# Kernel optimization log

Measured on AMD Instinct MI355X. Metric: run time of the kernel, lower is better.

## Reference

```python
import jax, jax.numpy as jnp
import numpy as np

EPS = 1e-6  # matches torch nn.CosineSimilarity(eps=1e-6)

B, D, N, K = 128, 512, 500000, 3


def setup_inputs() -> dict:
    key = jax.random.key(0)
    k1, k2, k3 = jax.random.split(key, 3)
    query_r = jax.random.normal(k1, (B, D), dtype=jnp.float32)
    corpus_emb = jax.random.normal(k2, (N, D), dtype=jnp.float32)
    # stand-in for self.retriever.model.forward (projection to embedding space)
    W = jax.random.normal(k3, (D, D), dtype=jnp.float32) / np.sqrt(D)
    return {"query_r": query_r, "corpus_emb": corpus_emb, "W": W, "k": K}


def _l2_normalize(x):
    # torch CosineSimilarity clamps the norm at eps, not norm+eps
    n = jnp.sqrt(jnp.sum(x * x, axis=-1, keepdims=True))
    return x / jnp.maximum(n, EPS)


def reference(query_r, corpus_emb, W, k):
    # retriever projection: query = retriever.model.forward(query_r)
    query = query_r @ W                      # [B, D]
    qn = _l2_normalize(query)                # [B, D]
    cn = _l2_normalize(corpus_emb)           # [N, D]
    # fused replacement for the per-item python-loop cosine scan
    scores = jnp.einsum('bd,nd->bn', qn, cn)  # [B, N]
    # sort(reverse=True)[:k]  ==  top-k
    top_scores, top_idx = jax.lax.top_k(scores, k)  # [B, k], [B, k]
    return top_scores, top_idx
```

## Files before the change

kernel.cpp:

```cpp
#include <hip/hip_runtime.h>
#include <math.h>

#define B_Q   128
#define DIM   512
#define NCORP 500000
#define NTILES 31250
#define G_SCAN 512

typedef short short8 __attribute__((ext_vector_type(8)));
typedef float floatx4 __attribute__((ext_vector_type(4)));

__device__ __forceinline__ unsigned short bf16_rne(float x) {
    unsigned u = __float_as_uint(x);
    return (unsigned short)((u + 0x7FFFu + ((u >> 16) & 1u)) >> 16);
}

__device__ __forceinline__ unsigned pack2(float hi, float lo) {
    return __builtin_amdgcn_perm(__float_as_uint(hi), __float_as_uint(lo),
                                 0x07060302u);
}

__device__ __forceinline__ void ins3(float s, int id,
                                     float& b0, float& b1, float& b2,
                                     int& i0, int& i1, int& i2) {
    if (s > b0)      { b2 = b1; i2 = i1; b1 = b0; i1 = i0; b0 = s; i0 = id; }
    else if (s > b1) { b2 = b1; i2 = i1; b1 = s;  i1 = id; }
    else if (s > b2) { b2 = s;  i2 = id; }
}

__device__ __forceinline__ void ins2(float s, int id,
                                     float& b0, float& b1, int& i0, int& i1) {
    if (s > b0)      { b1 = b0; i1 = i0; b0 = s; i0 = id; }
    else if (s > b1) { b1 = s;  i1 = id; }
}

__device__ __forceinline__ void ins8(float s, int id, float* bs, int* bi) {
#pragma unroll
    for (int j = 0; j < 8; ++j) {
        if (s > bs[j]) {
            float tf = bs[j]; int tx = bi[j];
            bs[j] = s; bi[j] = id; s = tf; id = tx;
        }
    }
}

__global__ void proj_kernel(const float* __restrict__ qr,
                            const float* __restrict__ W,
                            float* __restrict__ qn,
                            unsigned short* __restrict__ qfrag) {
    __shared__ float qrow[DIM];
    __shared__ float red[256];
    const int b = blockIdx.x;
    const int t = threadIdx.x;

    qrow[t]       = qr[b * DIM + t];
    qrow[t + 256] = qr[b * DIM + t + 256];
    __syncthreads();

    float acc0 = 0.f, acc1 = 0.f;
#pragma unroll 8
    for (int k = 0; k < DIM; ++k) {
        const float q = qrow[k];
        acc0 = fmaf(q, W[k * DIM + t],       acc0);
        acc1 = fmaf(q, W[k * DIM + t + 256], acc1);
    }

    red[t] = acc0 * acc0 + acc1 * acc1;
    __syncthreads();
    for (int s = 128; s > 0; s >>= 1) {
        if (t < s) red[t] += red[t + s];
        __syncthreads();
    }
    const float inv = 1.0f / fmaxf(sqrtf(red[0]), 1e-6f);

    const int qg = b >> 4, q15 = b & 15;
#pragma unroll
    for (int half = 0; half < 2; ++half) {
        const int d = t + half * 256;
        const float x = (half == 0 ? acc0 : acc1) * inv;
        qn[b * DIM + d] = x;
        const int kc = d >> 5, kk = d & 31, g = kk >> 3, e = kk & 7;
        qfrag[(size_t)kc * 4096 + qg * 512 + (g * 16 + q15) * 8 + e] = bf16_rne(x);
    }
}

__global__ __launch_bounds__(512, 4) void scan_kernel(
        const float* __restrict__ corpus,
        const unsigned short* __restrict__ qfrag,
        float* __restrict__ cand_s,
        int*   __restrict__ cand_i) {
    __shared__ __align__(16) unsigned char smem[32768];

    const int t = threadIdx.x;
    const int w = t >> 6, l = t & 63;
    const int h = l >> 4, q15 = l & 15;

    short8 qreg[16];
#pragma unroll
    for (int kc = 0; kc < 16; ++kc)
        qreg[kc] = *(const short8*)(qfrag + (size_t)kc * 4096 + w * 512 + l * 8);

    int goff[4], lby[4];
#pragma unroll
    for (int p = 0; p < 4; ++p) {
        const int i4 = p * 512 + t;
        const int r  = i4 >> 7;
        const int c4 = i4 & 127;
        const int kc = c4 >> 3, g = (c4 >> 1) & 3, e0 = (c4 & 1) * 4;
        goff[p] = i4 * 4;
        lby[p]  = kc * 1024 + (((g * 16 + r) ^ (kc & 7)) << 4) + e0 * 2;
    }

    const int b = blockIdx.x;
    const int tstart = b * 61 + (b < 18 ? b : 18);
    const int tcount = 61 + (b < 18 ? 1 : 0);
    const float* seg = corpus + (size_t)tstart * 8192;

    float ts0 = -1e30f, ts1 = -1e30f;
    int   ti0 = 0, ti1 = 0;

    float4 rr[4];
#pragma unroll
    for (int p = 0; p < 4; ++p) rr[p] = *(const float4*)(seg + goff[p]);

#pragma unroll 1
    for (int T = 0; T < tcount; ++T) {
        unsigned char* bb = smem + (T & 1) * 16384;

#pragma unroll
        for (int p = 0; p < 4; ++p) {
            uint2 d;
            d.x = pack2(rr[p].y, rr[p].x);
            d.y = pack2(rr[p].w, rr[p].z);
            *(uint2*)(bb + lby[p]) = d;
        }
        {
            const int Tn = (T + 1 < tcount) ? T + 1 : T;
            const float* src = seg + (size_t)Tn * 8192;
#pragma unroll
            for (int p = 0; p < 4; ++p) rr[p] = *(const float4*)(src + goff[p]);
        }
        __builtin_amdgcn_sched_barrier(0);
        asm volatile("s_waitcnt lgkmcnt(0)" ::: "memory");
        __builtin_amdgcn_s_barrier();
        __builtin_amdgcn_sched_barrier(0);

        floatx4 acc  = {0.f, 0.f, 0.f, 0.f};
        floatx4 accN = {0.f, 0.f, 0.f, 0.f};
#pragma unroll
        for (int kc = 0; kc < 16; ++kc) {
            const short8 a = *(const short8*)(bb + kc * 1024 +
                                              ((l ^ (kc & 7)) << 4));
            accN = __builtin_amdgcn_mfma_f32_16x16x32_bf16(a, a, accN, 0, 0, 0);
            acc  = __builtin_amdgcn_mfma_f32_16x16x32_bf16(a, qreg[kc], acc, 0, 0, 0);
        }

        const int grow = (tstart + T) * 16;
#pragma unroll
        for (int reg = 0; reg < 4; ++reg) {
            const float nrm = __shfl(accN[reg], h * 20 + reg, 64);
            const float inv = 1.0f / fmaxf(sqrtf(nrm), 1e-6f);
            ins2(acc[reg] * inv, grow + h * 4 + reg, ts0, ts1, ti0, ti1);
        }
    }

    __syncthreads();
    float* msc = (float*)smem;
    int*   mid = (int*)(smem + 4096);
    {
        const int myq = w * 16 + q15;
        msc[(myq * 4 + h) * 2 + 0] = ts0;  mid[(myq * 4 + h) * 2 + 0] = ti0;
        msc[(myq * 4 + h) * 2 + 1] = ts1;  mid[(myq * 4 + h) * 2 + 1] = ti1;
    }
    __syncthreads();
    if (t < B_Q) {
        float b0 = -1e30f, b1 = -1e30f, b2 = -1e30f;
        int   i0 = 0, i1 = 0, i2 = 0;
        for (int e = 0; e < 8; ++e)
            ins3(msc[t * 8 + e], mid[t * 8 + e], b0, b1, b2, i0, i1, i2);
        const size_t base = ((size_t)blockIdx.x * B_Q + t) * 3;
        cand_s[base + 0] = b0; cand_s[base + 1] = b1; cand_s[base + 2] = b2;
        cand_i[base + 0] = i0; cand_i[base + 1] = i1; cand_i[base + 2] = i2;
    }
}

__global__ void merge_topk_kernel(const float* __restrict__ cand_s,
                                  const int*   __restrict__ cand_i,
                                  int nblk,
                                  float* __restrict__ topT_s,
                                  int*   __restrict__ topT_i) {
    __shared__ float ls[256 * 8];
    __shared__ int   li[256 * 8];
    const int q = blockIdx.x;
    const int t = threadIdx.x;

    float bs[8]; int bi[8];
#pragma unroll
    for (int j = 0; j < 8; ++j) { bs[j] = -1e30f; bi[j] = -1; }

    for (int blk = t; blk < nblk; blk += 256) {
        const size_t base = ((size_t)blk * B_Q + q) * 3;
#pragma unroll
        for (int j = 0; j < 3; ++j)
            ins8(cand_s[base + j], cand_i[base + j], bs, bi);
    }
#pragma unroll
    for (int j = 0; j < 8; ++j) { ls[t * 8 + j] = bs[j]; li[t * 8 + j] = bi[j]; }
    __syncthreads();

    for (int s = 128; s > 0; s >>= 1) {
        if (t < s) {
#pragma unroll
            for (int j = 0; j < 8; ++j)
                ins8(ls[(t + s) * 8 + j], li[(t + s) * 8 + j], bs, bi);
#pragma unroll
            for (int j = 0; j < 8; ++j) { ls[t * 8 + j] = bs[j]; li[t * 8 + j] = bi[j]; }
        }
        __syncthreads();
    }
    if (t == 0) {
#pragma unroll
        for (int j = 0; j < 8; ++j) { topT_s[q * 8 + j] = bs[j]; topT_i[q * 8 + j] = bi[j]; }
    }
}

__global__ void rescore_kernel(const float* __restrict__ corpus,
                               const float* __restrict__ qn,
                               const int*   __restrict__ topT_i,
                               float* __restrict__ out) {
    __shared__ float qrow[DIM];
    __shared__ float sc[8];
    const int q = blockIdx.x;
    const int t = threadIdx.x;
    const int g = t >> 5;
    const int lane = t & 31;

    qrow[t]       = qn[q * DIM + t];
    qrow[t + 256] = qn[q * DIM + t + 256];
    __syncthreads();

    const int r = topT_i[q * 8 + g];
    float d = 0.f, n = 0.f;
    if (r >= 0) {
        const float* row = corpus + (size_t)r * DIM;
        for (int j = lane; j < DIM; j += 32) {
            const float c = row[j];
            d = fmaf(qrow[j], c, d);
            n = fmaf(c, c, n);
        }
    }
#pragma unroll
    for (int m = 16; m > 0; m >>= 1) {
        d += __shfl_xor(d, m);
        n += __shfl_xor(n, m);
    }
    if (lane == 0)
        sc[g] = (r >= 0) ? d / fmaxf(sqrtf(n), 1e-6f) : -1e30f;
    __syncthreads();

    if (t == 0) {
        float b0 = -1e30f, b1 = -1e30f, b2 = -1e30f;
        int   i0 = 0, i1 = 0, i2 = 0;
#pragma unroll
        for (int e = 0; e < 8; ++e)
            ins3(sc[e], topT_i[q * 8 + e], b0, b1, b2, i0, i1, i2);
        out[q * 3 + 0] = b0;
        out[q * 3 + 1] = b1;
        out[q * 3 + 2] = b2;
        out[B_Q * 3 + q * 3 + 0] = (float)i0;
        out[B_Q * 3 + q * 3 + 1] = (float)i1;
        out[B_Q * 3 + q * 3 + 2] = (float)i2;
    }
}

extern "C" void kernel_launch(void* const* d_in, const int* in_sizes, int n_in,
                              void* d_out, int out_size, void* d_ws, size_t ws_size,
                              hipStream_t stream) {
    const float* qr     = (const float*)d_in[0];
    const float* corpus = (const float*)d_in[1];
    const float* W      = (const float*)d_in[2];

    float* out = (float*)d_out;
    char*  ws  = (char*)d_ws;

    float*          qn     = (float*)ws;
    unsigned short* qfrag  = (unsigned short*)(ws + 262144);
    float*          topT_s = (float*)(ws + 393216);
    int*            topT_i = (int*)(ws + 397312);
    const size_t head = 401408;

    float* cand_s = (float*)(ws + head);
    int*   cand_i = (int*)(ws + head + (size_t)G_SCAN * B_Q * 3 * sizeof(float));

    proj_kernel<<<B_Q, 256, 0, stream>>>(qr, W, qn, qfrag);
    scan_kernel<<<G_SCAN, 512, 0, stream>>>(corpus, qfrag, cand_s, cand_i);
    merge_topk_kernel<<<B_Q, 256, 0, stream>>>(cand_s, cand_i, G_SCAN, topT_s, topT_i);
    rescore_kernel<<<B_Q, 256, 0, stream>>>(corpus, qn, topT_i, out);
}
```

Baseline: 372.7 us.

## Stage corpus tiles into LDS via direct global_load_lds and compute norms in fp32

Replaces the register round-trip (global load to registers, bf16 pack, LDS store) with asynchronous global_load_lds transfers of raw fp32 tiles into double-buffered, XOR-swizzled LDS. Each wave then reads fp32 from LDS, packs to bf16 for the score MFMA, and computes row norms with scalar fp32 FMAs plus shuffles, dropping the norm MFMA. This doubles LDS use to 64KB per block, which can lower occupancy. It also adds an extra barrier per tile and more LDS read bandwidth and VALU work per tile.

```diff
diff --git a/kernel.cpp b/kernel.cpp
--- a/kernel.cpp
+++ b/kernel.cpp
@@ -18,6 +18,12 @@
 __device__ __forceinline__ unsigned pack2(float hi, float lo) {
     return __builtin_amdgcn_perm(__float_as_uint(hi), __float_as_uint(lo),
                                  0x07060302u);
+}
+
+__device__ __forceinline__ void gload16(const float* g, float* l) {
+    __builtin_amdgcn_global_load_lds(
+        (const __attribute__((address_space(1))) unsigned*)g,
+        (__attribute__((address_space(3))) unsigned*)l, 16, 0, 0);
 }
 
 __device__ __forceinline__ void ins3(float s, int id,
@@ -89,7 +95,7 @@
         const unsigned short* __restrict__ qfrag,
         float* __restrict__ cand_s,
         int*   __restrict__ cand_i) {
-    __shared__ __align__(16) unsigned char smem[32768];
+    __shared__ __align__(16) unsigned char smem[65536];
 
     const int t = threadIdx.x;
     const int w = t >> 6, l = t & 63;
@@ -100,69 +106,80 @@
     for (int kc = 0; kc < 16; ++kc)
         qreg[kc] = *(const short8*)(qfrag + (size_t)kc * 4096 + w * 512 + l * 8);
 
-    int goff[4], lby[4];
-#pragma unroll
-    for (int p = 0; p < 4; ++p) {
-        const int i4 = p * 512 + t;
-        const int r  = i4 >> 7;
-        const int c4 = i4 & 127;
-        const int kc = c4 >> 3, g = (c4 >> 1) & 3, e0 = (c4 & 1) * 4;
-        goff[p] = i4 * 4;
-        lby[p]  = kc * 1024 + (((g * 16 + r) ^ (kc & 7)) << 4) + e0 * 2;
+    int srcoff[4];
+#pragma unroll
+    for (int i = 0; i < 4; ++i) {
+        const int row = w * 2 + (i >> 1);
+        const int gc  = (((i & 1) * 64) + l) ^ (row & 7);
+        srcoff[i] = row * 2048 + gc * 16;
     }
 
     const int b = blockIdx.x;
     const int tstart = b * 61 + (b < 18 ? b : 18);
     const int tcount = 61 + (b < 18 ? 1 : 0);
-    const float* seg = corpus + (size_t)tstart * 8192;
+    const unsigned char* segB = (const unsigned char*)corpus +
+                                (size_t)tstart * 32768;
+
+    const int rbase = q15 * 2048;
+    const int r7 = q15 & 7;
 
     float ts0 = -1e30f, ts1 = -1e30f;
     int   ti0 = 0, ti1 = 0;
 
-    float4 rr[4];
-#pragma unroll
-    for (int p = 0; p < 4; ++p) rr[p] = *(const float4*)(seg + goff[p]);
+#define STAGE(T, BUF) do {                                                     \
+        const unsigned char* _s = segB + (size_t)(T) * 32768;                  \
+        _Pragma("unroll")                                                      \
+        for (int i = 0; i < 4; ++i)                                            \
+            gload16((const float*)(_s + srcoff[i]),                            \
+                    (float*)(smem + (BUF) * 32768 + w * 4096 + i * 1024));     \
+    } while (0)
+
+    STAGE(0, 0);
 
 #pragma unroll 1
     for (int T = 0; T < tcount; ++T) {
-        unsigned char* bb = smem + (T & 1) * 16384;
-
-#pragma unroll
-        for (int p = 0; p < 4; ++p) {
-            uint2 d;
-            d.x = pack2(rr[p].y, rr[p].x);
-            d.y = pack2(rr[p].w, rr[p].z);
-            *(uint2*)(bb + lby[p]) = d;
-        }
+        const int par = T & 1;
         {
             const int Tn = (T + 1 < tcount) ? T + 1 : T;
-            const float* src = seg + (size_t)Tn * 8192;
-#pragma unroll
-            for (int p = 0; p < 4; ++p) rr[p] = *(const float4*)(src + goff[p]);
+            STAGE(Tn, par ^ 1);
         }
         __builtin_amdgcn_sched_barrier(0);
-        asm volatile("s_waitcnt lgkmcnt(0)" ::: "memory");
+        asm volatile("s_waitcnt vmcnt(4)" ::: "memory");
         __builtin_amdgcn_s_barrier();
         __builtin_amdgcn_sched_barrier(0);
 
-        floatx4 acc  = {0.f, 0.f, 0.f, 0.f};
-        floatx4 accN = {0.f, 0.f, 0.f, 0.f};
+        const unsigned char* bb = smem + par * 32768;
+        floatx4 acc = {0.f, 0.f, 0.f, 0.f};
+        float nsq = 0.f;
 #pragma unroll
         for (int kc = 0; kc < 16; ++kc) {
-            const short8 a = *(const short8*)(bb + kc * 1024 +
-                                              ((l ^ (kc & 7)) << 4));
-            accN = __builtin_amdgcn_mfma_f32_16x16x32_bf16(a, a, accN, 0, 0, 0);
-            acc  = __builtin_amdgcn_mfma_f32_16x16x32_bf16(a, qreg[kc], acc, 0, 0, 0);
-        }
+            const int g0 = (kc * 8 + h * 2) ^ r7;
+            const int g1 = (kc * 8 + h * 2 + 1) ^ r7;
+            const float4 f0 = *(const float4*)(bb + rbase + g0 * 16);
+            const float4 f1 = *(const float4*)(bb + rbase + g1 * 16);
+            nsq += f0.x*f0.x + f0.y*f0.y + f0.z*f0.z + f0.w*f0.w
+                 + f1.x*f1.x + f1.y*f1.y + f1.z*f1.z + f1.w*f1.w;
+            uint4 ap;
+            ap.x = pack2(f0.y, f0.x); ap.y = pack2(f0.w, f0.z);
+            ap.z = pack2(f1.y, f1.x); ap.w = pack2(f1.w, f1.z);
+            const short8 a = __builtin_bit_cast(short8, ap);
+            acc = __builtin_amdgcn_mfma_f32_16x16x32_bf16(a, qreg[kc], acc, 0, 0, 0);
+        }
+
+        float n = nsq;
+        n += __shfl_xor(n, 16); n += __shfl_xor(n, 32);
+        const float invn = 1.0f / fmaxf(sqrtf(n), 1e-6f);
 
         const int grow = (tstart + T) * 16;
 #pragma unroll
         for (int reg = 0; reg < 4; ++reg) {
-            const float nrm = __shfl(accN[reg], h * 20 + reg, 64);
-            const float inv = 1.0f / fmaxf(sqrtf(nrm), 1e-6f);
-            ins2(acc[reg] * inv, grow + h * 4 + reg, ts0, ts1, ti0, ti1);
-        }
-    }
+            const int m = h * 4 + reg;
+            const float iv = __shfl(invn, m, 64);
+            ins2(acc[reg] * iv, grow + m, ts0, ts1, ti0, ti1);
+        }
+        __builtin_amdgcn_s_barrier();
+    }
+#undef STAGE
 
     __syncthreads();
     float* msc = (float*)smem;
```

After: 554.9 us. +48.9%, slower.
